# Optimization experiments

Hardware: AMD Instinct MI355X
Metric: run time of the kernel (lower is better)

## Reference

```python
import jax, jax.numpy as jnp
import numpy as np

# dims
T, B, C_IN, C_OUT, NE, RD = 256, 8, 256, 256, 64, 64
TAU = 1.0          # gumbel_tau
COMMIT = 0.25      # commitment_scale
KMEANS = 1.0       # train_embeddings_scale
IMP = 30.0         # imp_loss_scale (hard-coded in module)


def setup_inputs() -> dict:
    key = jax.random.key(0)
    k0, k1, k2, k3 = jax.random.split(key, 4)
    a = np.sqrt(6.0) / (C_IN + C_OUT)  # dynamic_init_method==1 uniform bound
    return {
        "x": jax.random.normal(k0, (T, B, C_IN), jnp.float32),
        "map_w": jax.random.normal(k1, (RD, C_IN), jnp.float32) / np.sqrt(C_IN),
        "map_b": jnp.zeros((RD,), jnp.float32),
        "centroids": jax.random.normal(k2, (NE, RD), jnp.float32) * 0.5,
        "pw_w": jax.random.uniform(k3, (NE, C_OUT * C_IN), jnp.float32, -a, a),
        "pw_B": jnp.zeros((1, 1, C_OUT), jnp.float32),
    }


def reference(x, map_w, map_b, centroids, pw_w, pw_B):
    # key projection: (T*B, RD)
    k = x.reshape(T * B, C_IN) @ map_w.T + map_b
    # squared euclidean distances to centroids: (T*B, NE)
    d = (jnp.sum(k * k, axis=1, keepdims=True)
         + jnp.sum(centroids * centroids, axis=1)
         - 2.0 * (k @ centroids.T))
    # gumbel-softmax (soft, training path) with fixed noise
    g = jax.random.gumbel(jax.random.key(42), d.shape, d.dtype)
    resp = jax.nn.softmax((-d + g) / TAU, axis=-1)  # (T*B, NE)
    quantized = resp @ centroids                    # (T*B, RD)
    commitment_loss = jnp.mean((k - jax.lax.stop_gradient(quantized)) ** 2)
    kmeans_loss = jnp.mean((jax.lax.stop_gradient(k) - quantized) ** 2)
    importance = resp.sum(axis=0)                   # (NE,)
    imp_loss = jnp.std(importance, ddof=1) / jnp.mean(importance)
    loss = COMMIT * commitment_loss + IMP * imp_loss + KMEANS * kmeans_loss
    # soft expert-weight combine then per-token matvec
    w = (resp @ pw_w).reshape(T, B, C_OUT, C_IN)    # (T,B,out,in)
    out = jnp.einsum('tboi,tbi->tbo', w, x) + pw_B  # constant-bias mode
    return out, loss
```

## Files before the change

kernel.cpp:

```cpp
#include <hip/hip_runtime.h>
#include <stdint.h>

#define CIN   256
#define COUT  256
#define NE    64
#define RD    64
#define NTOK  2048

typedef __attribute__((ext_vector_type(8))) short bf16x8;
typedef __attribute__((ext_vector_type(4))) float f32x4;

__device__ inline unsigned short f2bf(float f) {
    uint32_t u = __float_as_uint(f);
    uint32_t r = (u + 0x7FFFu + ((u >> 16) & 1u)) >> 16;
    return (unsigned short)r;
}

__device__ inline float wave_sum(float v) {
    #pragma unroll
    for (int m = 1; m < 64; m <<= 1) v += __shfl_xor(v, m, 64);
    return v;
}
__device__ inline float wave_max(float v) {
    #pragma unroll
    for (int m = 1; m < 64; m <<= 1) v = fmaxf(v, __shfl_xor(v, m, 64));
    return v;
}

__device__ inline uint32_t rotl32(uint32_t v, int d) { return (v << d) | (v >> (32 - d)); }

__device__ inline void threefry_0_42(uint32_t c0, uint32_t c1, uint32_t& o0, uint32_t& o1) {
    const uint32_t ks0 = 0u, ks1 = 42u, ks2 = 0u ^ 42u ^ 0x1BD11BDAu;
    uint32_t x0 = c0 + ks0, x1 = c1 + ks1;
#define TF_R(r) { x0 += x1; x1 = rotl32(x1, r); x1 ^= x0; }
    TF_R(13) TF_R(15) TF_R(26) TF_R(6)
    x0 += ks1; x1 += ks2 + 1u;
    TF_R(17) TF_R(29) TF_R(16) TF_R(24)
    x0 += ks2; x1 += ks0 + 2u;
    TF_R(13) TF_R(15) TF_R(26) TF_R(6)
    x0 += ks0; x1 += ks1 + 3u;
    TF_R(17) TF_R(29) TF_R(16) TF_R(24)
    x0 += ks1; x1 += ks2 + 4u;
    TF_R(13) TF_R(15) TF_R(26) TF_R(6)
    x0 += ks2; x1 += ks0 + 5u;
#undef TF_R
    o0 = x0; o1 = x1;
}

__global__ __launch_bounds__(256) void pack_b_kernel(const float* __restrict__ pw,
                                                     unsigned short* __restrict__ Bp) {
    int G = blockIdx.x * 256 + threadIdx.x;
    int tile = G >> 10, qg = G & 1023;
    int e = tile >> 3, kc = tile & 7;
    int row = qg >> 2, gp = qg & 3;
    int k16 = gp ^ ((row >> 1) & 3);
    const float* s = pw + ((size_t)e << 16) + (row << 8) + (kc << 5) + (k16 << 3);
    float4 v0 = *(const float4*)s;
    float4 v1 = *(const float4*)(s + 4);
    ushort4 a, b;
    a.x = f2bf(v0.x); a.y = f2bf(v0.y); a.z = f2bf(v0.z); a.w = f2bf(v0.w);
    b.x = f2bf(v1.x); b.y = f2bf(v1.y); b.z = f2bf(v1.z); b.w = f2bf(v1.w);
    *(ushort4*)(Bp + ((size_t)G << 3)) = a;
    *(ushort4*)(Bp + ((size_t)G << 3) + 4) = b;
}

__global__ __launch_bounds__(256) void vq_kernel(
    const float* __restrict__ x, const float* __restrict__ mw,
    const float* __restrict__ mb, const float* __restrict__ cent,
    float* __restrict__ resp_out, float* __restrict__ commit_out)
{
    __shared__ float xs[4][CIN];
    __shared__ float cs[NE][RD + 1];
    __shared__ float ksh[4][RD];
    __shared__ float rs[4][NE];

    const int tid = threadIdx.x;
    const int w   = tid >> 6;
    const int t   = tid & 63;
    const int tb  = (blockIdx.x << 2) + w;

    ((float4*)xs[w])[t] = ((const float4*)(x + (size_t)tb * CIN))[t];
    #pragma unroll
    for (int j = 0; j < 4; ++j) {
        int fidx = (j << 8) + tid;
        float4 v = ((const float4*)cent)[fidx];
        int row = fidx >> 4, c0 = (fidx & 15) << 2;
        cs[row][c0] = v.x; cs[row][c0 + 1] = v.y; cs[row][c0 + 2] = v.z; cs[row][c0 + 3] = v.w;
    }
    __syncthreads();

    float kr = mb[t];
    const float4* mwr = (const float4*)(mw + (size_t)t * CIN);
    #pragma unroll 8
    for (int j = 0; j < 64; ++j) {
        float4 wv = mwr[j];
        kr += wv.x * xs[w][(j << 2)] + wv.y * xs[w][(j << 2) + 1]
            + wv.z * xs[w][(j << 2) + 2] + wv.w * xs[w][(j << 2) + 3];
    }
    ksh[w][t] = kr;
    float kk = wave_sum(kr * kr);
    __syncthreads();

    float cc = 0.f, dt = 0.f;
    #pragma unroll 8
    for (int r = 0; r < 64; ++r) {
        float cv = cs[t][r];
        cc += cv * cv;
        dt += ksh[w][r] * cv;
    }
    float d = kk + cc - 2.f * dt;

    uint32_t fidx = (uint32_t)((tb << 6) + t);
    uint32_t cnt  = fidx < 65536u ? fidx : fidx - 65536u;
    uint32_t o0, o1;
    threefry_0_42(cnt, cnt + 65536u, o0, o1);
    uint32_t bits = fidx < 65536u ? o0 : o1;
    float uf = __uint_as_float((bits >> 9) | 0x3f800000u) - 1.0f;
    uf = fmaxf(uf, 1.17549435e-38f);
    float g = -logf(-logf(uf));

    float sv = g - d;
    float mx = wave_max(sv);
    float p  = expf(sv - mx);
    float ps = wave_sum(p);
    float rv = p / ps;
    resp_out[(tb << 6) + t] = rv;
    rs[w][t] = rv;
    __syncthreads();

    float q = 0.f;
    #pragma unroll 8
    for (int e2 = 0; e2 < 64; ++e2) q += rs[w][e2] * cs[e2][t];
    float df = kr - q;
    float sq = wave_sum(df * df);
    if (t == 0) commit_out[tb] = sq;
}

__global__ __launch_bounds__(256) void loss_part_kernel(const float* __restrict__ resp,
                                                        const float* __restrict__ commit_part,
                                                        float* __restrict__ imp_p,
                                                        float* __restrict__ cm_p)
{
    const int b = blockIdx.x, t = threadIdx.x;
    const int e = t & 63, grp = t >> 6;
    float s = 0.f;
    #pragma unroll
    for (int j = 0; j < 16; ++j)
        s += resp[(size_t)((b << 6) + (grp << 4) + j) * 64 + e];
    __shared__ float part[4][64];
    part[grp][e] = s;
    __syncthreads();
    if (t < 64) {
        float v = part[0][t] + part[1][t] + part[2][t] + part[3][t];
        imp_p[(b << 6) + t] = v;
        float cm = commit_part[(b << 6) + t];
        cm = wave_sum(cm);
        if (t == 0) cm_p[b] = cm;
    }
}

__global__ __launch_bounds__(64) void loss_final_kernel(const float* __restrict__ imp_p,
                                                        const float* __restrict__ cm_p,
                                                        float* __restrict__ loss_out)
{
    const int t = threadIdx.x;
    float imp = 0.f;
    #pragma unroll
    for (int b = 0; b < 32; ++b) imp += imp_p[(b << 6) + t];
    float ct = (t < 32) ? cm_p[t] : 0.f;
    ct = wave_sum(ct);
    float tot  = wave_sum(imp);
    float mean = tot * (1.0f / 64.f);
    float dv   = imp - mean;
    float var  = wave_sum(dv * dv) * (1.0f / 63.f);
    if (t == 0) {
        float mse = ct * (1.0f / (float)(NTOK * RD));
        float imp_loss = sqrtf(var) / mean;
        loss_out[0] = (0.25f + 1.0f) * mse + 30.0f * imp_loss;
    }
}

__device__ inline void stage_b32(char* dst, const char* src, int w, int lane) {
    #pragma unroll
    for (int i = 0; i < 8; ++i) {
        const int off = (w << 13) + (i << 10);
        __builtin_amdgcn_global_load_lds(
            (const __attribute__((address_space(1))) unsigned int*)(src + off + (lane << 4)),
            (__attribute__((address_space(3))) unsigned int*)(dst + off), 16, 0, 0);
    }
}

__global__ __launch_bounds__(256) void gemm_kernel(
    const float* __restrict__ x, const float* __restrict__ resp,
    const unsigned short* __restrict__ Bp, float* __restrict__ partial)
{
    __shared__ char lds[81920];
    char* As  = lds;
    char* Bs0 = lds + 16384;
    char* Bs1 = lds + 49152;

    const int tid  = threadIdx.x;
    const int lane = tid & 63;
    const int w    = tid >> 6;
    const int lo   = lane & 15, kq = lane >> 4;
    const int g    = blockIdx.x & 7;
    const int m0   = (blockIdx.x >> 3) << 5;

    {
        const float4* x4 = (const float4*)(x + (size_t)m0 * CIN);
        #pragma unroll
        for (int it = 0; it < 8; ++it) {
            int i = (it << 8) + tid;
            float4 v = x4[i];
            int row = i >> 6, k4 = i & 63;
            int slot = k4 >> 1, half = k4 & 1;
            ushort4 u;
            u.x = f2bf(v.x); u.y = f2bf(v.y); u.z = f2bf(v.z); u.w = f2bf(v.w);
            *(ushort4*)(As + (row << 9) + ((slot ^ (row & 7)) << 4) + (half << 3)) = u;
        }
    }

    const char* bsrc = (const char*)Bp + ((size_t)g << 20);
    stage_b32(Bs0, bsrc, w, lane);
    __syncthreads();

    f32x4 P[2][4] = {};
    f32x4 O[2][4] = {};
    const f32x4 z = {};

    char* cur = Bs0;
    char* nxt = Bs1;

    for (int p = 0; p < 32; ++p) {
        if (p + 1 < 32) stage_b32(nxt, bsrc + ((size_t)(p + 1) << 15), w, lane);

        #pragma unroll
        for (int sub = 0; sub < 2; ++sub) {
            const int kc = ((p & 3) << 1) + sub;
            char* bt = cur + (sub << 14);
            bf16x8 af[2], bfr[4];
            #pragma unroll
            for (int mi = 0; mi < 2; ++mi) {
                int row = (mi << 4) + lo;
                af[mi] = *(const bf16x8*)(As + (row << 9) + ((((kc << 2) + kq) ^ (row & 7)) << 4));
            }
            #pragma unroll
            for (int ni = 0; ni < 4; ++ni) {
                int row = (w << 6) + (ni << 4) + lo;
                bfr[ni] = *(const bf16x8*)(bt + (row << 6) + ((kq ^ ((row >> 1) & 3)) << 4));
            }
            #pragma unroll
            for (int mi = 0; mi < 2; ++mi)
                #pragma unroll
                for (int ni = 0; ni < 4; ++ni)
                    P[mi][ni] = __builtin_amdgcn_mfma_f32_16x16x32_bf16(
                        af[mi], bfr[ni], P[mi][ni], 0, 0, 0);
        }

        if ((p & 3) == 3) {
            const int e = (g << 3) + (p >> 2);
            float r[2][4];
            const float* rb = resp + ((size_t)(m0 + (kq << 2)) << 6) + e;
            #pragma unroll
            for (int mi = 0; mi < 2; ++mi)
                #pragma unroll
                for (int j = 0; j < 4; ++j)
                    r[mi][j] = rb[(size_t)((mi << 4) + j) << 6];
            #pragma unroll
            for (int mi = 0; mi < 2; ++mi)
                #pragma unroll
                for (int ni = 0; ni < 4; ++ni) {
                    #pragma unroll
                    for (int j = 0; j < 4; ++j)
                        O[mi][ni][j] += r[mi][j] * P[mi][ni][j];
                    P[mi][ni] = z;
                }
        }
        __syncthreads();
        char* tmp = cur; cur = nxt; nxt = tmp;
    }

    float* pout = partial + ((size_t)g << 19)
                + ((size_t)(m0 + (kq << 2)) << 8) + (w << 6) + lo;
    #pragma unroll
    for (int mi = 0; mi < 2; ++mi)
        #pragma unroll
        for (int j = 0; j < 4; ++j) {
            float* pr = pout + ((size_t)((mi << 4) + j) << 8);
            #pragma unroll
            for (int ni = 0; ni < 4; ++ni)
                pr[ni << 4] = O[mi][ni][j];
        }
}

__global__ __launch_bounds__(256) void reduce_kernel(const float* __restrict__ partial,
                                                     const float* __restrict__ bias,
                                                     float* __restrict__ out)
{
    int idx = blockIdx.x * 256 + threadIdx.x;
    float4 s = ((const float4*)bias)[idx & 63];
    #pragma unroll
    for (int g = 0; g < 8; ++g) {
        float4 v = ((const float4*)partial)[((size_t)g << 17) + idx];
        s.x += v.x; s.y += v.y; s.z += v.z; s.w += v.w;
    }
    ((float4*)out)[idx] = s;
}

extern "C" void kernel_launch(void* const* d_in, const int* in_sizes, int n_in,
                              void* d_out, int out_size, void* d_ws, size_t ws_size,
                              hipStream_t stream)
{
    const float* x     = (const float*)d_in[0];
    const float* map_w = (const float*)d_in[1];
    const float* map_b = (const float*)d_in[2];
    const float* cent  = (const float*)d_in[3];
    const float* pw_w  = (const float*)d_in[4];
    const float* pw_B  = (const float*)d_in[5];
    float* out = (float*)d_out;

    char* ws = (char*)d_ws;
    float* resp        = (float*)ws;
    float* commit      = (float*)(ws + 524288);
    float* imp_p       = (float*)(ws + 540672);
    float* cm_p        = (float*)(ws + 557056);
    unsigned short* Bp = (unsigned short*)(ws + (1u << 20));
    float* partial     = (float*)(ws + (10u << 20));

    pack_b_kernel<<<2048, 256, 0, stream>>>(pw_w, Bp);
    vq_kernel<<<512, 256, 0, stream>>>(x, map_w, map_b, cent, resp, commit);
    gemm_kernel<<<512, 256, 0, stream>>>(x, resp, Bp, partial);
    reduce_kernel<<<512, 256, 0, stream>>>(partial, pw_B, out);
    loss_part_kernel<<<32, 256, 0, stream>>>(resp, commit, imp_p, cm_p);
    loss_final_kernel<<<1, 64, 0, stream>>>(imp_p, cm_p, out + NTOK * COUT);
}
```

Measured before the change: 68.29 us.

## Retile expert GEMM with register-resident A and fuse small kernels

The pack kernel is merged into the VQ kernel as extra blocks, and the reduce and loss-partial kernels are merged, cutting two launches. The GEMM is retiled to 128-row by 64-column tiles with the A operand held in registers, a 4-deep ring of 4KB B stages driven by explicit vmcnt waits, responsibilities cached in LDS, and a small LDS footprint with launch bounds for two blocks per CU. The aim is better latency hiding and less LDS traffic per MFMA. The risks are higher register pressure from keeping A in registers and the hand-written waitcnt and barrier scheme.

Result: slower. 91.74 us (+34.3%).

```diff
diff --git a/kernel.cpp b/kernel.cpp
--- a/kernel.cpp
+++ b/kernel.cpp
@@ -47,24 +47,8 @@
     o0 = x0; o1 = x1;
 }
 
-__global__ __launch_bounds__(256) void pack_b_kernel(const float* __restrict__ pw,
-                                                     unsigned short* __restrict__ Bp) {
-    int G = blockIdx.x * 256 + threadIdx.x;
-    int tile = G >> 10, qg = G & 1023;
-    int e = tile >> 3, kc = tile & 7;
-    int row = qg >> 2, gp = qg & 3;
-    int k16 = gp ^ ((row >> 1) & 3);
-    const float* s = pw + ((size_t)e << 16) + (row << 8) + (kc << 5) + (k16 << 3);
-    float4 v0 = *(const float4*)s;
-    float4 v1 = *(const float4*)(s + 4);
-    ushort4 a, b;
-    a.x = f2bf(v0.x); a.y = f2bf(v0.y); a.z = f2bf(v0.z); a.w = f2bf(v0.w);
-    b.x = f2bf(v1.x); b.y = f2bf(v1.y); b.z = f2bf(v1.z); b.w = f2bf(v1.w);
-    *(ushort4*)(Bp + ((size_t)G << 3)) = a;
-    *(ushort4*)(Bp + ((size_t)G << 3) + 4) = b;
-}
-
-__global__ __launch_bounds__(256) void vq_kernel(
+__global__ __launch_bounds__(256) void vq_pack_kernel(
+    const float* __restrict__ pw, unsigned short* __restrict__ Bp,
     const float* __restrict__ x, const float* __restrict__ mw,
     const float* __restrict__ mb, const float* __restrict__ cent,
     float* __restrict__ resp_out, float* __restrict__ commit_out)
@@ -75,9 +59,29 @@
     __shared__ float rs[4][NE];
 
     const int tid = threadIdx.x;
-    const int w   = tid >> 6;
-    const int t   = tid & 63;
-    const int tb  = (blockIdx.x << 2) + w;
+
+    if (blockIdx.x >= 512) {
+        int G = (blockIdx.x - 512) * 256 + tid;
+        int tile = G >> 8, qg = G & 255;
+        int ct = tile >> 9, g = (tile >> 6) & 7, p = tile & 63;
+        int e = (g << 3) + (p >> 3), kc = p & 7;
+        int n = qg >> 2, gp = qg & 3;
+        int k16 = gp ^ ((n >> 1) & 3);
+        int o = (ct << 6) + n;
+        const float* s = pw + ((size_t)e << 16) + (o << 8) + (kc << 5) + (k16 << 3);
+        float4 v0 = *(const float4*)s;
+        float4 v1 = *(const float4*)(s + 4);
+        ushort4 a, b;
+        a.x = f2bf(v0.x); a.y = f2bf(v0.y); a.z = f2bf(v0.z); a.w = f2bf(v0.w);
+        b.x = f2bf(v1.x); b.y = f2bf(v1.y); b.z = f2bf(v1.z); b.w = f2bf(v1.w);
+        *(ushort4*)(Bp + ((size_t)G << 3)) = a;
+        *(ushort4*)(Bp + ((size_t)G << 3) + 4) = b;
+        return;
+    }
+
+    const int w  = tid >> 6;
+    const int t  = tid & 63;
+    const int tb = (blockIdx.x << 2) + w;
 
     ((float4*)xs[w])[t] = ((const float4*)(x + (size_t)tb * CIN))[t];
     #pragma unroll
@@ -117,13 +121,13 @@
     uint32_t bits = fidx < 65536u ? o0 : o1;
     float uf = __uint_as_float((bits >> 9) | 0x3f800000u) - 1.0f;
     uf = fmaxf(uf, 1.17549435e-38f);
-    float g = -logf(-logf(uf));
-
-    float sv = g - d;
+    float g2 = -logf(-logf(uf));
+
+    float sv = g2 - d;
     float mx = wave_max(sv);
-    float p  = expf(sv - mx);
-    float ps = wave_sum(p);
-    float rv = p / ps;
+    float pz = expf(sv - mx);
+    float ps = wave_sum(pz);
+    float rv = pz / ps;
     resp_out[(tb << 6) + t] = rv;
     rs[w][t] = rv;
     __syncthreads();
@@ -136,18 +140,151 @@
     if (t == 0) commit_out[tb] = sq;
 }
 
-__global__ __launch_bounds__(256) void loss_part_kernel(const float* __restrict__ resp,
-                                                        const float* __restrict__ commit_part,
-                                                        float* __restrict__ imp_p,
-                                                        float* __restrict__ cm_p)
-{
-    const int b = blockIdx.x, t = threadIdx.x;
+__device__ inline void stage1(const char* src, char* dst, int lane) {
+    __builtin_amdgcn_global_load_lds(
+        (const __attribute__((address_space(1))) unsigned int*)(src + (lane << 4)),
+        (__attribute__((address_space(3))) unsigned int*)dst, 16, 0, 0);
+}
+
+__global__ __launch_bounds__(256, 2) void gemm_kernel(
+    const float* __restrict__ x, const float* __restrict__ resp,
+    const unsigned short* __restrict__ Bp, float* __restrict__ partial)
+{
+    __shared__ char Bb[16384];
+    __shared__ float rsh[128][8];
+
+    const int tid  = threadIdx.x;
+    const int lane = tid & 63;
+    const int w    = tid >> 6;
+    const int lo   = lane & 15, kq = lane >> 4;
+    const int bid  = blockIdx.x;
+    const int g    = bid & 7, ct = (bid >> 3) & 3, mt = bid >> 5;
+    const int m0   = mt << 7;
+
+    {
+        int idx = tid << 2;
+        int row = idx >> 3, e0 = idx & 7;
+        float4 rv = *(const float4*)(resp + ((size_t)(m0 + row) << 6) + (g << 3) + e0);
+        *(float4*)(&rsh[row][e0]) = rv;
+    }
+
+    bf16x8 af[2][8];
+    {
+        const float* xb = x + ((size_t)(m0 + (w << 5) + lo) << 8) + (kq << 3);
+        #pragma unroll
+        for (int mi = 0; mi < 2; ++mi)
+            #pragma unroll
+            for (int kc = 0; kc < 8; ++kc) {
+                const float* s = xb + (mi << 12) + (kc << 5);
+                float4 v0 = *(const float4*)s;
+                float4 v1 = *(const float4*)(s + 4);
+                bf16x8 bv;
+                bv[0] = (short)f2bf(v0.x); bv[1] = (short)f2bf(v0.y);
+                bv[2] = (short)f2bf(v0.z); bv[3] = (short)f2bf(v0.w);
+                bv[4] = (short)f2bf(v1.x); bv[5] = (short)f2bf(v1.y);
+                bv[6] = (short)f2bf(v1.z); bv[7] = (short)f2bf(v1.w);
+                af[mi][kc] = bv;
+            }
+    }
+
+    const char* bsrc = (const char*)Bp + ((size_t)((ct << 3) + g) << 18);
+
+    asm volatile("s_waitcnt vmcnt(0)" ::: "memory");
+    asm volatile("s_waitcnt lgkmcnt(0)" ::: "memory");
+
+    stage1(bsrc + (0 << 12) + (w << 10), Bb + ((0 & 3) << 12) + (w << 10), lane);
+    stage1(bsrc + (1 << 12) + (w << 10), Bb + ((1 & 3) << 12) + (w << 10), lane);
+    stage1(bsrc + (2 << 12) + (w << 10), Bb + ((2 & 3) << 12) + (w << 10), lane);
+
+    f32x4 P[2][4] = {};
+    f32x4 O[2][4] = {};
+    const f32x4 z = {};
+
+    for (int p = 0; p < 64; ++p) {
+        if (p < 62)       asm volatile("s_waitcnt vmcnt(2)" ::: "memory");
+        else if (p == 62) asm volatile("s_waitcnt vmcnt(1)" ::: "memory");
+        else              asm volatile("s_waitcnt vmcnt(0)" ::: "memory");
+        asm volatile("s_barrier" ::: "memory");
+
+        char* bt = Bb + ((p & 3) << 12);
+        bf16x8 bfr[4];
+        #pragma unroll
+        for (int ni = 0; ni < 4; ++ni) {
+            int n = (ni << 4) + lo;
+            bfr[ni] = *(const bf16x8*)(bt + (n << 6) + ((kq ^ ((n >> 1) & 3)) << 4));
+        }
+
+        if (p + 3 < 64)
+            stage1(bsrc + ((size_t)(p + 3) << 12) + (w << 10),
+                   Bb + (((p + 3) & 3) << 12) + (w << 10), lane);
+
+        const int kc = p & 7;
+        #pragma unroll
+        for (int mi = 0; mi < 2; ++mi)
+            #pragma unroll
+            for (int ni = 0; ni < 4; ++ni)
+                P[mi][ni] = __builtin_amdgcn_mfma_f32_16x16x32_bf16(
+                    af[mi][kc], bfr[ni], P[mi][ni], 0, 0, 0);
+
+        if ((p & 7) == 7) {
+            const int el = p >> 3;
+            #pragma unroll
+            for (int mi = 0; mi < 2; ++mi) {
+                float r[4];
+                #pragma unroll
+                for (int j = 0; j < 4; ++j)
+                    r[j] = rsh[(w << 5) + (mi << 4) + (kq << 2) + j][el];
+                #pragma unroll
+                for (int ni = 0; ni < 4; ++ni) {
+                    #pragma unroll
+                    for (int j = 0; j < 4; ++j)
+                        O[mi][ni][j] += r[j] * P[mi][ni][j];
+                    P[mi][ni] = z;
+                }
+            }
+        }
+    }
+
+    float* pout = partial + ((size_t)g << 19)
+                + ((size_t)(m0 + (w << 5) + (kq << 2)) << 8) + (ct << 6) + lo;
+    #pragma unroll
+    for (int mi = 0; mi < 2; ++mi)
+        #pragma unroll
+        for (int j = 0; j < 4; ++j) {
+            float* pr = pout + ((size_t)((mi << 4) + j) << 8);
+            #pragma unroll
+            for (int ni = 0; ni < 4; ++ni)
+                pr[ni << 4] = O[mi][ni][j];
+        }
+}
+
+__global__ __launch_bounds__(256) void reduce_loss_kernel(
+    const float* __restrict__ partial, const float* __restrict__ bias,
+    float* __restrict__ out, const float* __restrict__ resp,
+    const float* __restrict__ commit_part, float* __restrict__ imp_p,
+    float* __restrict__ cm_p)
+{
+    __shared__ float part[4][64];
+    const int t = threadIdx.x;
+
+    if (blockIdx.x < 512) {
+        int idx = blockIdx.x * 256 + t;
+        float4 s = ((const float4*)bias)[idx & 63];
+        #pragma unroll
+        for (int g = 0; g < 8; ++g) {
+            float4 v = ((const float4*)partial)[((size_t)g << 17) + idx];
+            s.x += v.x; s.y += v.y; s.z += v.z; s.w += v.w;
+        }
+        ((float4*)out)[idx] = s;
+        return;
+    }
+
+    const int b = blockIdx.x - 512;
     const int e = t & 63, grp = t >> 6;
     float s = 0.f;
     #pragma unroll
     for (int j = 0; j < 16; ++j)
         s += resp[(size_t)((b << 6) + (grp << 4) + j) * 64 + e];
-    __shared__ float part[4][64];
     part[grp][e] = s;
     __syncthreads();
     if (t < 64) {
@@ -180,133 +317,6 @@
     }
 }
 
-__device__ inline void stage_b32(char* dst, const char* src, int w, int lane) {
-    #pragma unroll
-    for (int i = 0; i < 8; ++i) {
-        const int off = (w << 13) + (i << 10);
-        __builtin_amdgcn_global_load_lds(
-            (const __attribute__((address_space(1))) unsigned int*)(src + off + (lane << 4)),
-            (__attribute__((address_space(3))) unsigned int*)(dst + off), 16, 0, 0);
-    }
-}
-
-__global__ __launch_bounds__(256) void gemm_kernel(
-    const float* __restrict__ x, const float* __restrict__ resp,
-    const unsigned short* __restrict__ Bp, float* __restrict__ partial)
-{
-    __shared__ char lds[81920];
-    char* As  = lds;
-    char* Bs0 = lds + 16384;
-    char* Bs1 = lds + 49152;
-
-    const int tid  = threadIdx.x;
-    const int lane = tid & 63;
-    const int w    = tid >> 6;
-    const int lo   = lane & 15, kq = lane >> 4;
-    const int g    = blockIdx.x & 7;
-    const int m0   = (blockIdx.x >> 3) << 5;
-
-    {
-        const float4* x4 = (const float4*)(x + (size_t)m0 * CIN);
-        #pragma unroll
-        for (int it = 0; it < 8; ++it) {
-            int i = (it << 8) + tid;
-            float4 v = x4[i];
-            int row = i >> 6, k4 = i & 63;
-            int slot = k4 >> 1, half = k4 & 1;
-            ushort4 u;
-            u.x = f2bf(v.x); u.y = f2bf(v.y); u.z = f2bf(v.z); u.w = f2bf(v.w);
-            *(ushort4*)(As + (row << 9) + ((slot ^ (row & 7)) << 4) + (half << 3)) = u;
-        }
-    }
-
-    const char* bsrc = (const char*)Bp + ((size_t)g << 20);
-    stage_b32(Bs0, bsrc, w, lane);
-    __syncthreads();
-
-    f32x4 P[2][4] = {};
-    f32x4 O[2][4] = {};
-    const f32x4 z = {};
-
-    char* cur = Bs0;
-    char* nxt = Bs1;
-
-    for (int p = 0; p < 32; ++p) {
-        if (p + 1 < 32) stage_b32(nxt, bsrc + ((size_t)(p + 1) << 15), w, lane);
-
-        #pragma unroll
-        for (int sub = 0; sub < 2; ++sub) {
-            const int kc = ((p & 3) << 1) + sub;
-            char* bt = cur + (sub << 14);
-            bf16x8 af[2], bfr[4];
-            #pragma unroll
-            for (int mi = 0; mi < 2; ++mi) {
-                int row = (mi << 4) + lo;
-                af[mi] = *(const bf16x8*)(As + (row << 9) + ((((kc << 2) + kq) ^ (row & 7)) << 4));
-            }
-            #pragma unroll
-            for (int ni = 0; ni < 4; ++ni) {
-                int row = (w << 6) + (ni << 4) + lo;
-                bfr[ni] = *(const bf16x8*)(bt + (row << 6) + ((kq ^ ((row >> 1) & 3)) << 4));
-            }
-            #pragma unroll
-            for (int mi = 0; mi < 2; ++mi)
-                #pragma unroll
-                for (int ni = 0; ni < 4; ++ni)
-                    P[mi][ni] = __builtin_amdgcn_mfma_f32_16x16x32_bf16(
-                        af[mi], bfr[ni], P[mi][ni], 0, 0, 0);
-        }
-
-        if ((p & 3) == 3) {
-            const int e = (g << 3) + (p >> 2);
-            float r[2][4];
-            const float* rb = resp + ((size_t)(m0 + (kq << 2)) << 6) + e;
-            #pragma unroll
-            for (int mi = 0; mi < 2; ++mi)
-                #pragma unroll
-                for (int j = 0; j < 4; ++j)
-                    r[mi][j] = rb[(size_t)((mi << 4) + j) << 6];
-            #pragma unroll
-            for (int mi = 0; mi < 2; ++mi)
-                #pragma unroll
-                for (int ni = 0; ni < 4; ++ni) {
-                    #pragma unroll
-                    for (int j = 0; j < 4; ++j)
-                        O[mi][ni][j] += r[mi][j] * P[mi][ni][j];
-                    P[mi][ni] = z;
-                }
-        }
-        __syncthreads();
-        char* tmp = cur; cur = nxt; nxt = tmp;
-    }
-
-    float* pout = partial + ((size_t)g << 19)
-                + ((size_t)(m0 + (kq << 2)) << 8) + (w << 6) + lo;
-    #pragma unroll
-    for (int mi = 0; mi < 2; ++mi)
-        #pragma unroll
-        for (int j = 0; j < 4; ++j) {
-            float* pr = pout + ((size_t)((mi << 4) + j) << 8);
-            #pragma unroll
-            for (int ni = 0; ni < 4; ++ni)
-                pr[ni << 4] = O[mi][ni][j];
-        }
-}
-
-__global__ __launch_bounds__(256) void reduce_kernel(const float* __restrict__ partial,
-                                                     const float* __restrict__ bias,
-                                                     float* __restrict__ out)
-{
-    int idx = blockIdx.x * 256 + threadIdx.x;
-    float4 s = ((const float4*)bias)[idx & 63];
-    #pragma unroll
-    for (int g = 0; g < 8; ++g) {
-        float4 v = ((const float4*)partial)[((size_t)g << 17) + idx];
-        s.x += v.x; s.y += v.y; s.z += v.z; s.w += v.w;
-    }
-    ((float4*)out)[idx] = s;
-}
-
 extern "C" void kernel_launch(void* const* d_in, const int* in_sizes, int n_in,
                               void* d_out, int out_size, void* d_ws, size_t ws_size,
                               hipStream_t stream)
@@ -327,10 +337,8 @@
     unsigned short* Bp = (unsigned short*)(ws + (1u << 20));
     float* partial     = (float*)(ws + (10u << 20));
 
-    pack_b_kernel<<<2048, 256, 0, stream>>>(pw_w, Bp);
-    vq_kernel<<<512, 256, 0, stream>>>(x, map_w, map_b, cent, resp, commit);
+    vq_pack_kernel<<<2560, 256, 0, stream>>>(pw_w, Bp, x, map_w, map_b, cent, resp, commit);
     gemm_kernel<<<512, 256, 0, stream>>>(x, resp, Bp, partial);
-    reduce_kernel<<<512, 256, 0, stream>>>(partial, pw_B, out);
-    loss_part_kernel<<<32, 256, 0, stream>>>(resp, commit, imp_p, cm_p);
+    reduce_loss_kernel<<<544, 256, 0, stream>>>(partial, pw_B, out, resp, commit, imp_p, cm_p);
     loss_final_kernel<<<1, 64, 0, stream>>>(imp_p, cm_p, out + NTOK * COUT);
 }
```
